# Kernel optimization log

Hardware: AMD Instinct MI355X
Metric: run time of the kernel (lower is better)

## Reference

```python
import jax, jax.numpy as jnp
import numpy as np

N, E, H, B = 10000, 320000, 256, 128
ATOM_TYPES, BOND_TYPES = 100, 5


def _timestep_embed(t, dim):
    # Sinusoidal timestep embedding, matching the torch _embed_timestep
    half = dim // 2
    freq = jnp.exp(jnp.arange(half, dtype=jnp.float32) * (-np.log(10000.0) / (half - 1)))
    ang = t[:, None] * freq[None, :]  # [B, half]
    return jnp.concatenate([jnp.sin(ang), jnp.cos(ang)], axis=1)  # [B, dim]


def setup_inputs() -> dict:
    key = jax.random.key(0)
    ks = jax.random.split(key, 9)
    s = 0.02
    return {
        "node_features": jax.random.normal(ks[0], (N, H), jnp.float32),
        "pos_pred": jax.random.normal(ks[1], (N, 3), jnp.float32),
        "edge_index": jax.random.randint(ks[2], (2, E), 0, N),
        "batch": jnp.sort(jax.random.randint(ks[3], (N,), 0, B)),
        "t_discrete": jax.random.uniform(ks[4], (B,), jnp.float32) * 1000.0,
        "atom_w1": jax.random.normal(ks[5], (H, H), jnp.float32) * s,
        "atom_b1": jnp.zeros((H,), jnp.float32),
        "atom_w2": jax.random.normal(ks[6], (H, ATOM_TYPES), jnp.float32) * s,
        "atom_b2": jnp.zeros((ATOM_TYPES,), jnp.float32),
        "bond_w1": jax.random.normal(ks[7], (2 * H, H), jnp.float32) * s,
        "bond_b1": jnp.zeros((H,), jnp.float32),
        "bond_w2": jax.random.normal(ks[8], (H, BOND_TYPES), jnp.float32) * s,
        "bond_b2": jnp.zeros((BOND_TYPES,), jnp.float32),
    }


def reference(node_features, pos_pred, edge_index, batch, t_discrete,
              atom_w1, atom_b1, atom_w2, atom_b2,
              bond_w1, bond_b1, bond_w2, bond_b2):
    # timestep embed + per-node broadcast-gather
    t_emb = _timestep_embed(t_discrete, node_features.shape[1])  # [B, H]
    h = node_features + t_emb[batch]  # [N, H]

    # atom denoiser MLP
    atom_logits = jax.nn.relu(h @ atom_w1 + atom_b1) @ atom_w2 + atom_b2  # [N, ATOM_TYPES]

    # gather node pairs, concat, bond denoiser MLP
    row, col = edge_index[0], edge_index[1]
    e = jnp.concatenate([h[row], h[col]], axis=-1)  # [E, 2H]
    bond_logits = jax.nn.relu(e @ bond_w1 + bond_b1) @ bond_w2 + bond_b2  # [E, BOND_TYPES]

    return pos_pred, atom_logits, bond_logits, node_features
```

## Files before the change

### kernel.cpp

```cpp
#include <hip/hip_runtime.h>
#include <hip/hip_bf16.h>

typedef __bf16 bf16x8 __attribute__((ext_vector_type(8)));
typedef float  f32x4  __attribute__((ext_vector_type(4)));

#define N_NODES 10000
#define N_EDGES 320000

#define WS_TEMB   0u
#define WS_H      131072u
#define WS_W1AT   5251072u
#define WS_W2AT   5382144u
#define WS_W1BT   5439488u
#define WS_W2BT   5701632u

__global__ void prep_kernel(const float* __restrict__ aw1, const float* __restrict__ aw2,
                            const float* __restrict__ bw1, const float* __restrict__ bw2,
                            const float* __restrict__ t,
                            __hip_bfloat16* __restrict__ W1a, __hip_bfloat16* __restrict__ W2a,
                            __hip_bfloat16* __restrict__ W1b, __hip_bfloat16* __restrict__ W2b,
                            float* __restrict__ temb)
{
    int blk = blockIdx.x;
    if (blk < 256) {
        int i = blk * 256 + threadIdx.x;
        int n = i >> 8, k = i & 255;
        W1a[i] = __float2bfloat16(aw1[k * 256 + n]);
    } else if (blk < 368) {
        int i = (blk - 256) * 256 + threadIdx.x;
        int n = i >> 8, k = i & 255;
        W2a[i] = __float2bfloat16(n < 100 ? aw2[k * 100 + n] : 0.0f);
    } else if (blk < 880) {
        int i = (blk - 368) * 256 + threadIdx.x;
        int n = i >> 9, k = i & 511;
        W1b[i] = __float2bfloat16(bw1[k * 256 + n]);
    } else if (blk < 896) {
        int i = (blk - 880) * 256 + threadIdx.x;
        int n = i >> 8, k = i & 255;
        W2b[i] = __float2bfloat16(n < 5 ? bw2[k * 5 + n] : 0.0f);
    } else {
        int q = blk - 896;
        int b = q * 2 + (threadIdx.x >> 7);
        int i = threadIdx.x & 127;
        float freq = expf((float)i * (-9.210340371976184f / 127.0f));
        float ang  = t[b] * freq;
        temb[b * 256 + i]       = sinf(ang);
        temb[b * 256 + 128 + i] = cosf(ang);
    }
}

__global__ void h_kernel(const float* __restrict__ nf, const int* __restrict__ batch,
                         const float* __restrict__ temb, __hip_bfloat16* __restrict__ hb,
                         float* __restrict__ out_nf,
                         const float4* __restrict__ pos_src, float4* __restrict__ pos_dst)
{
    int blk = blockIdx.x;
    if (blk >= 1250) {
        int j = (blk - 1250) * 256 + threadIdx.x;
        if (j < 7500) pos_dst[j] = pos_src[j];
        return;
    }
    int i = blk * 256 + threadIdx.x;
    int n = i >> 5;
    int c = (i & 31) << 3;
    const float4* p = (const float4*)(nf + (size_t)n * 256 + c);
    float4 v0 = p[0], v1 = p[1];
    int b = batch[n];
    const float4* q = (const float4*)(temb + (size_t)b * 256 + c);
    float4 t0 = q[0], t1 = q[1];
    union { int4 i4; __hip_bfloat16 h[8]; } u;
    u.h[0] = __float2bfloat16(v0.x + t0.x);
    u.h[1] = __float2bfloat16(v0.y + t0.y);
    u.h[2] = __float2bfloat16(v0.z + t0.z);
    u.h[3] = __float2bfloat16(v0.w + t0.w);
    u.h[4] = __float2bfloat16(v1.x + t1.x);
    u.h[5] = __float2bfloat16(v1.y + t1.y);
    u.h[6] = __float2bfloat16(v1.z + t1.z);
    u.h[7] = __float2bfloat16(v1.w + t1.w);
    *(int4*)((char*)hb + (size_t)n * 512 + (size_t)c * 2) = u.i4;
    float4* o = (float4*)(out_nf + (size_t)n * 256 + c);
    o[0] = v0; o[1] = v1;
}

__device__ __forceinline__ void gload16(const void* g, void* l)
{
    __builtin_amdgcn_global_load_lds(
        (const __attribute__((address_space(1))) unsigned int*)g,
        (__attribute__((address_space(3))) unsigned int*)l, 16, 0, 0);
}

template<int KSTEPS, bool GATHER, int N2F, int N2REAL>
__global__ __launch_bounds__(256, 2) void mlp_kernel(
    const __hip_bfloat16* __restrict__ hb,
    const __hip_bfloat16* __restrict__ w1t,
    const __hip_bfloat16* __restrict__ w2t,
    const float* __restrict__ b1,
    const float* __restrict__ b2,
    const int*  __restrict__ eidx,
    int M,
    float* __restrict__ out)
{
    extern __shared__ char lds[];
    const int t  = threadIdx.x;
    const int w  = t >> 6;
    const int l  = t & 63;
    const int m0 = blockIdx.x * 64;

    const int swz = (((l & 7) ^ (l >> 3)) << 4);

    const char* hbase = (const char*)hb;
    int srcA[2][2];
    #pragma unroll
    for (int i = 0; i < 2; ++i) {
        int am = i * 32 + w * 8 + (l >> 3);
        if (GATHER) {
            int e = m0 + am;
            srcA[i][0] = eidx[e] * 512 + swz;
            srcA[i][1] = eidx[N_EDGES + e] * 512 + swz;
        } else {
            int r = m0 + am; if (r > M - 1) r = M - 1;
            srcA[i][0] = r * 512 + swz;
            srcA[i][1] = srcA[i][0];
        }
    }
    const char* w1base = (const char*)w1t;
    int srcB[8];
    #pragma unroll
    for (int i = 0; i < 8; ++i) {
        int n = i * 32 + w * 8 + (l >> 3);
        srcB[i] = n * (KSTEPS * 128) + swz;
    }

    f32x4 acc[4][4];
    const f32x4 zero4 = {0.f, 0.f, 0.f, 0.f};
    #pragma unroll
    for (int i = 0; i < 4; ++i)
        #pragma unroll
        for (int j = 0; j < 4; ++j) acc[i][j] = zero4;

    auto STAGE = [&](int ks, char* buf) {
        int koffA = (GATHER ? (ks & (KSTEPS / 2 - 1)) : ks) * 128;
        int side  = (GATHER && ks >= KSTEPS / 2) ? 1 : 0;
        #pragma unroll
        for (int i = 0; i < 2; ++i)
            gload16(hbase + (long)(srcA[i][side] + koffA), buf + (i * 4 + w) * 1024);
        int koffB = ks * 128;
        #pragma unroll
        for (int i = 0; i < 8; ++i)
            gload16(w1base + (long)(srcB[i] + koffB), buf + 8192 + (i * 4 + w) * 1024);
    };

    STAGE(0, lds);
    __syncthreads();

    #pragma unroll
    for (int ks = 0; ks < KSTEPS; ++ks) {
        char* cur = lds + (ks & 1) * 40960;
        if (ks + 1 < KSTEPS) STAGE(ks + 1, lds + ((ks + 1) & 1) * 40960);
        bf16x8 af[4][2];
        #pragma unroll
        for (int mi = 0; mi < 4; ++mi)
            #pragma unroll
            for (int k1 = 0; k1 < 2; ++k1)
                af[mi][k1] = *(const bf16x8*)(cur + (mi * 16 + (l & 15)) * 128 +
                                              (((k1 * 4 + (l >> 4)) ^ (l & 7)) << 4));
        #pragma unroll
        for (int ni = 0; ni < 4; ++ni) {
            #pragma unroll
            for (int k1 = 0; k1 < 2; ++k1) {
                bf16x8 bfr = *(const bf16x8*)(cur + 8192 + (w * 64 + ni * 16 + (l & 15)) * 128 +
                                              (((k1 * 4 + (l >> 4)) ^ (l & 7)) << 4));
                #pragma unroll
                for (int mi = 0; mi < 4; ++mi)
                    acc[mi][ni] = __builtin_amdgcn_mfma_f32_16x16x32_bf16(af[mi][k1], bfr, acc[mi][ni], 0, 0, 0);
            }
        }
        __syncthreads();
    }

    __hip_bfloat16* Hid = (__hip_bfloat16*)lds;
    {
        float b1v[4];
        #pragma unroll
        for (int ni = 0; ni < 4; ++ni) b1v[ni] = b1[w * 64 + ni * 16 + (l & 15)];
        #pragma unroll
        for (int mi = 0; mi < 4; ++mi)
            #pragma unroll
            for (int ni = 0; ni < 4; ++ni)
                #pragma unroll
                for (int r = 0; r < 4; ++r) {
                    int m = mi * 16 + (l >> 4) * 4 + r;
                    int n = w * 64 + ni * 16 + (l & 15);
                    float v = acc[mi][ni][r] + b1v[ni];
                    Hid[m * 264 + n] = __float2bfloat16(fmaxf(v, 0.0f));
                }
    }
    __syncthreads();

    f32x4 acc2[N2F];
    #pragma unroll
    for (int i = 0; i < N2F; ++i) acc2[i] = zero4;
    const char* w2base = (const char*)w2t;
    #pragma unroll
    for (int ks = 0; ks < 8; ++ks) {
        bf16x8 a2 = *(const bf16x8*)(lds + (w * 16 + (l & 15)) * 528 + ks * 64 + (l >> 4) * 16);
        #pragma unroll
        for (int nf2 = 0; nf2 < N2F; ++nf2) {
            bf16x8 b2f = *(const bf16x8*)(w2base + (nf2 * 16 + (l & 15)) * 512 + ks * 64 + (l >> 4) * 16);
            acc2[nf2] = __builtin_amdgcn_mfma_f32_16x16x32_bf16(a2, b2f, acc2[nf2], 0, 0, 0);
        }
    }
    #pragma unroll
    for (int nf2 = 0; nf2 < N2F; ++nf2) {
        int n = nf2 * 16 + (l & 15);
        if (n < N2REAL) {
            float b2v = b2[n];
            #pragma unroll
            for (int r = 0; r < 4; ++r) {
                int m  = w * 16 + (l >> 4) * 4 + r;
                int gm = m0 + m;
                if (gm < M)
                    out[(long)gm * N2REAL + n] = acc2[nf2][r] + b2v;
            }
        }
    }
}

extern "C" void kernel_launch(void* const* d_in, const int* in_sizes, int n_in,
                              void* d_out, int out_size, void* d_ws, size_t ws_size,
                              hipStream_t stream)
{
    const float* node_features = (const float*)d_in[0];
    const float* pos_pred      = (const float*)d_in[1];
    const int*   edge_index    = (const int*)d_in[2];
    const int*   batch         = (const int*)d_in[3];
    const float* t_disc        = (const float*)d_in[4];
    const float* atom_w1       = (const float*)d_in[5];
    const float* atom_b1       = (const float*)d_in[6];
    const float* atom_w2       = (const float*)d_in[7];
    const float* atom_b2       = (const float*)d_in[8];
    const float* bond_w1       = (const float*)d_in[9];
    const float* bond_b1       = (const float*)d_in[10];
    const float* bond_w2       = (const float*)d_in[11];
    const float* bond_b2       = (const float*)d_in[12];

    char* ws = (char*)d_ws;
    float*          temb = (float*)(ws + WS_TEMB);
    __hip_bfloat16* hbf  = (__hip_bfloat16*)(ws + WS_H);
    __hip_bfloat16* W1at = (__hip_bfloat16*)(ws + WS_W1AT);
    __hip_bfloat16* W2at = (__hip_bfloat16*)(ws + WS_W2AT);
    __hip_bfloat16* W1bt = (__hip_bfloat16*)(ws + WS_W1BT);
    __hip_bfloat16* W2bt = (__hip_bfloat16*)(ws + WS_W2BT);

    float* out      = (float*)d_out;
    float* out_pos  = out;
    float* out_atom = out + 30000;
    float* out_bond = out + 1030000;
    float* out_nf   = out + 2630000;

    prep_kernel<<<960, 256, 0, stream>>>(atom_w1, atom_w2, bond_w1, bond_w2, t_disc,
                                         W1at, W2at, W1bt, W2bt, temb);
    h_kernel<<<1280, 256, 0, stream>>>(node_features, batch, temb, hbf, out_nf,
                                       (const float4*)pos_pred, (float4*)out_pos);
    mlp_kernel<4, false, 7, 100><<<157, 256, 81920, stream>>>(
        hbf, W1at, W2at, atom_b1, atom_b2, nullptr, N_NODES, out_atom);
    mlp_kernel<8, true, 1, 5><<<5000, 256, 81920, stream>>>(
        hbf, W1bt, W2bt, bond_b1, bond_b2, edge_index, N_EDGES, out_bond);
}
```

Measured before the change: 220.8 us.

## Enlarge MLP block tile to 256 rows with 8 waves in 2x4 layout

Each MLP block now processes 256 rows instead of 64. It uses 512 threads arranged as 2x4 waves, each wave computing a 128x64 sub-tile. This reuses each staged W1 tile across four times as many rows, cutting weight traffic from global memory to LDS. The hidden tile is stored in LDS with an XOR swizzle, and the second GEMM gives each wave 32 rows. In exchange, LDS grows to 128KB per block, which allows only one block per CU. The register demand (128 accumulator registers) under launch_bounds(512,2) risks spilling, and the atom kernel drops to 40 blocks.

```diff
diff --git a/kernel.cpp b/kernel.cpp
--- a/kernel.cpp
+++ b/kernel.cpp
@@ -89,8 +89,8 @@
         (__attribute__((address_space(3))) unsigned int*)l, 16, 0, 0);
 }
 
-template<int KSTEPS, bool GATHER, int N2F, int N2REAL>
-__global__ __launch_bounds__(256, 2) void mlp_kernel(
+template<int NT, bool GATHER, int N2F, int N2REAL>
+__global__ __launch_bounds__(512, 2) void mlp_kernel(
     const __hip_bfloat16* __restrict__ hb,
     const __hip_bfloat16* __restrict__ w1t,
     const __hip_bfloat16* __restrict__ w2t,
@@ -101,18 +101,20 @@
     float* __restrict__ out)
 {
     extern __shared__ char lds[];
-    const int t  = threadIdx.x;
-    const int w  = t >> 6;
-    const int l  = t & 63;
-    const int m0 = blockIdx.x * 64;
-
-    const int swz = (((l & 7) ^ (l >> 3)) << 4);
+    const int t   = threadIdx.x;
+    const int wid = t >> 6;
+    const int l   = t & 63;
+    const int wm  = wid >> 2;
+    const int wn  = wid & 3;
+    const int m0  = blockIdx.x * 256;
+
+    const int swz = (((t & 7) ^ ((t >> 3) & 7)) << 4);
 
     const char* hbase = (const char*)hb;
-    int srcA[2][2];
-    #pragma unroll
-    for (int i = 0; i < 2; ++i) {
-        int am = i * 32 + w * 8 + (l >> 3);
+    int srcA[4][2];
+    #pragma unroll
+    for (int i = 0; i < 4; ++i) {
+        int am = i * 64 + (t >> 3);
         if (GATHER) {
             int e = m0 + am;
             srcA[i][0] = eidx[e] * 512 + swz;
@@ -124,90 +126,96 @@
         }
     }
     const char* w1base = (const char*)w1t;
-    int srcB[8];
-    #pragma unroll
-    for (int i = 0; i < 8; ++i) {
-        int n = i * 32 + w * 8 + (l >> 3);
-        srcB[i] = n * (KSTEPS * 128) + swz;
-    }
-
-    f32x4 acc[4][4];
-    const f32x4 zero4 = {0.f, 0.f, 0.f, 0.f};
+    int srcB[4];
     #pragma unroll
     for (int i = 0; i < 4; ++i)
-        #pragma unroll
-        for (int j = 0; j < 4; ++j) acc[i][j] = zero4;
+        srcB[i] = (i * 64 + (t >> 3)) * (NT * 128) + swz;
+
+    f32x4 acc[8][4];
+    #pragma unroll
+    for (int i = 0; i < 8; ++i)
+        #pragma unroll
+        for (int j = 0; j < 4; ++j) acc[i][j] = f32x4{0.f, 0.f, 0.f, 0.f};
 
     auto STAGE = [&](int ks, char* buf) {
-        int koffA = (GATHER ? (ks & (KSTEPS / 2 - 1)) : ks) * 128;
-        int side  = (GATHER && ks >= KSTEPS / 2) ? 1 : 0;
-        #pragma unroll
-        for (int i = 0; i < 2; ++i)
-            gload16(hbase + (long)(srcA[i][side] + koffA), buf + (i * 4 + w) * 1024);
+        int side  = (GATHER && ks >= NT / 2) ? 1 : 0;
+        int koffA = (GATHER ? (ks & (NT / 2 - 1)) : ks) * 128;
+        #pragma unroll
+        for (int i = 0; i < 4; ++i)
+            gload16(hbase + (long)(srcA[i][side] + koffA), buf + i * 8192 + wid * 1024);
         int koffB = ks * 128;
         #pragma unroll
-        for (int i = 0; i < 8; ++i)
-            gload16(w1base + (long)(srcB[i] + koffB), buf + 8192 + (i * 4 + w) * 1024);
+        for (int i = 0; i < 4; ++i)
+            gload16(w1base + (long)(srcB[i] + koffB), buf + 32768 + i * 8192 + wid * 1024);
     };
 
     STAGE(0, lds);
+
+    for (int kt = 0; kt < NT; ++kt) {
+        __syncthreads();
+        if (kt + 1 < NT) STAGE(kt + 1, lds + (((kt + 1) & 1) << 16));
+        const char* cur = lds + ((kt & 1) << 16);
+        #pragma unroll
+        for (int k1 = 0; k1 < 2; ++k1) {
+            const int jx = (k1 * 4 + (l >> 4)) ^ (l & 7);
+            bf16x8 af[8];
+            #pragma unroll
+            for (int mi = 0; mi < 8; ++mi) {
+                int r = wm * 128 + mi * 16 + (l & 15);
+                af[mi] = *(const bf16x8*)(cur + r * 128 + (jx << 4));
+            }
+            #pragma unroll
+            for (int ni = 0; ni < 4; ++ni) {
+                int rn = wn * 64 + ni * 16 + (l & 15);
+                bf16x8 bfr = *(const bf16x8*)(cur + 32768 + rn * 128 + (jx << 4));
+                #pragma unroll
+                for (int mi = 0; mi < 8; ++mi)
+                    acc[mi][ni] = __builtin_amdgcn_mfma_f32_16x16x32_bf16(af[mi], bfr, acc[mi][ni], 0, 0, 0);
+            }
+        }
+    }
+
     __syncthreads();
-
-    #pragma unroll
-    for (int ks = 0; ks < KSTEPS; ++ks) {
-        char* cur = lds + (ks & 1) * 40960;
-        if (ks + 1 < KSTEPS) STAGE(ks + 1, lds + ((ks + 1) & 1) * 40960);
-        bf16x8 af[4][2];
-        #pragma unroll
-        for (int mi = 0; mi < 4; ++mi)
-            #pragma unroll
-            for (int k1 = 0; k1 < 2; ++k1)
-                af[mi][k1] = *(const bf16x8*)(cur + (mi * 16 + (l & 15)) * 128 +
-                                              (((k1 * 4 + (l >> 4)) ^ (l & 7)) << 4));
-        #pragma unroll
-        for (int ni = 0; ni < 4; ++ni) {
-            #pragma unroll
-            for (int k1 = 0; k1 < 2; ++k1) {
-                bf16x8 bfr = *(const bf16x8*)(cur + 8192 + (w * 64 + ni * 16 + (l & 15)) * 128 +
-                                              (((k1 * 4 + (l >> 4)) ^ (l & 7)) << 4));
-                #pragma unroll
-                for (int mi = 0; mi < 4; ++mi)
-                    acc[mi][ni] = __builtin_amdgcn_mfma_f32_16x16x32_bf16(af[mi][k1], bfr, acc[mi][ni], 0, 0, 0);
-            }
-        }
-        __syncthreads();
-    }
-
-    __hip_bfloat16* Hid = (__hip_bfloat16*)lds;
     {
         float b1v[4];
         #pragma unroll
-        for (int ni = 0; ni < 4; ++ni) b1v[ni] = b1[w * 64 + ni * 16 + (l & 15)];
-        #pragma unroll
-        for (int mi = 0; mi < 4; ++mi)
+        for (int ni = 0; ni < 4; ++ni) b1v[ni] = b1[wn * 64 + ni * 16 + (l & 15)];
+        #pragma unroll
+        for (int mi = 0; mi < 8; ++mi)
             #pragma unroll
             for (int ni = 0; ni < 4; ++ni)
                 #pragma unroll
                 for (int r = 0; r < 4; ++r) {
-                    int m = mi * 16 + (l >> 4) * 4 + r;
-                    int n = w * 64 + ni * 16 + (l & 15);
-                    float v = acc[mi][ni][r] + b1v[ni];
-                    Hid[m * 264 + n] = __float2bfloat16(fmaxf(v, 0.0f));
+                    int m = wm * 128 + mi * 16 + (l >> 4) * 4 + r;
+                    int n = wn * 64 + ni * 16 + (l & 15);
+                    float v = fmaxf(acc[mi][ni][r] + b1v[ni], 0.0f);
+                    int byte = m * 512 + ((((n >> 3) ^ (m & 7)) << 4)) + ((n & 7) << 1);
+                    *(__hip_bfloat16*)(lds + byte) = __float2bfloat16(v);
                 }
     }
     __syncthreads();
 
-    f32x4 acc2[N2F];
-    #pragma unroll
-    for (int i = 0; i < N2F; ++i) acc2[i] = zero4;
+    f32x4 acc2[2][N2F];
+    #pragma unroll
+    for (int i = 0; i < 2; ++i)
+        #pragma unroll
+        for (int j = 0; j < N2F; ++j) acc2[i][j] = f32x4{0.f, 0.f, 0.f, 0.f};
     const char* w2base = (const char*)w2t;
     #pragma unroll
     for (int ks = 0; ks < 8; ++ks) {
-        bf16x8 a2 = *(const bf16x8*)(lds + (w * 16 + (l & 15)) * 528 + ks * 64 + (l >> 4) * 16);
+        const int jx2 = (ks * 4 + (l >> 4)) ^ (l & 7);
+        bf16x8 a2[2];
+        #pragma unroll
+        for (int mi2 = 0; mi2 < 2; ++mi2) {
+            int r2 = wid * 32 + mi2 * 16 + (l & 15);
+            a2[mi2] = *(const bf16x8*)(lds + r2 * 512 + (jx2 << 4));
+        }
         #pragma unroll
         for (int nf2 = 0; nf2 < N2F; ++nf2) {
             bf16x8 b2f = *(const bf16x8*)(w2base + (nf2 * 16 + (l & 15)) * 512 + ks * 64 + (l >> 4) * 16);
-            acc2[nf2] = __builtin_amdgcn_mfma_f32_16x16x32_bf16(a2, b2f, acc2[nf2], 0, 0, 0);
+            #pragma unroll
+            for (int mi2 = 0; mi2 < 2; ++mi2)
+                acc2[mi2][nf2] = __builtin_amdgcn_mfma_f32_16x16x32_bf16(a2[mi2], b2f, acc2[mi2][nf2], 0, 0, 0);
         }
     }
     #pragma unroll
@@ -216,12 +224,13 @@
         if (n < N2REAL) {
             float b2v = b2[n];
             #pragma unroll
-            for (int r = 0; r < 4; ++r) {
-                int m  = w * 16 + (l >> 4) * 4 + r;
-                int gm = m0 + m;
-                if (gm < M)
-                    out[(long)gm * N2REAL + n] = acc2[nf2][r] + b2v;
-            }
+            for (int mi2 = 0; mi2 < 2; ++mi2)
+                #pragma unroll
+                for (int r = 0; r < 4; ++r) {
+                    int gm = m0 + wid * 32 + mi2 * 16 + (l >> 4) * 4 + r;
+                    if (gm < M)
+                        out[(long)gm * N2REAL + n] = acc2[mi2][nf2][r] + b2v;
+                }
         }
     }
 }
@@ -262,8 +271,8 @@
                                          W1at, W2at, W1bt, W2bt, temb);
     h_kernel<<<1280, 256, 0, stream>>>(node_features, batch, temb, hbf, out_nf,
                                        (const float4*)pos_pred, (float4*)out_pos);
-    mlp_kernel<4, false, 7, 100><<<157, 256, 81920, stream>>>(
+    mlp_kernel<4, false, 7, 100><<<40, 512, 131072, stream>>>(
         hbf, W1at, W2at, atom_b1, atom_b2, nullptr, N_NODES, out_atom);
-    mlp_kernel<8, true, 1, 5><<<5000, 256, 81920, stream>>>(
+    mlp_kernel<8, true, 1, 5><<<1250, 512, 131072, stream>>>(
         hbf, W1bt, W2bt, bond_b1, bond_b2, edge_index, N_EDGES, out_bond);
 }
```

New measurement: 214.6 us. 2.8% less time.
